# Optimization experiments

Measured on AMD Instinct MI355X. Metric: run time of the kernel, lower is better.

Reference implementation:

```python
import jax, jax.numpy as jnp
import numpy as np

N_NODES = 100000


def gcn_conv(x, src, dst, W, b, n_nodes):
    # PyG GCNConv: h = X W; out[i] = sum_j norm_ij * h[j] + b, with self-loops
    # and symmetric normalization norm_ij = deg(i)^-1/2 * deg(j)^-1/2.
    h = x @ W  # [N, out]
    deg = jax.ops.segment_sum(jnp.ones_like(dst, dtype=h.dtype), dst, num_segments=n_nodes)
    dinv = jnp.where(deg > 0, jax.lax.rsqrt(deg), 0.0)
    norm = dinv[src] * dinv[dst]  # [E]
    msg = h[src] * norm[:, None]  # [E, out] gather + scale
    out = jax.ops.segment_sum(msg, dst, num_segments=n_nodes)  # scatter-add
    return out + b


def setup_inputs() -> dict:
    key = jax.random.key(0)
    k_x, k_e, k_w1, k_w2 = jax.random.split(key, 4)
    in_c, hid, out_c = 128, 64, 32
    x = jax.random.normal(k_x, (N_NODES, in_c), dtype=jnp.float32)
    edge_index = jax.random.randint(k_e, (2, 1600000), 0, N_NODES, dtype=jnp.int32)
    W1 = jax.random.normal(k_w1, (in_c, hid), dtype=jnp.float32) / np.sqrt(in_c)
    b1 = jnp.zeros((hid,), dtype=jnp.float32)
    W2 = jax.random.normal(k_w2, (hid, out_c), dtype=jnp.float32) / np.sqrt(hid)
    b2 = jnp.zeros((out_c,), dtype=jnp.float32)
    return {"x": x, "edge_index": edge_index, "W1": W1, "b1": b1, "W2": W2, "b2": b2}


def reference(x, edge_index, W1, b1, W2, b2):
    n = x.shape[0]
    # add self-loops (GCNConv default)
    loops = jnp.arange(n, dtype=edge_index.dtype)
    src = jnp.concatenate([edge_index[0], loops])
    dst = jnp.concatenate([edge_index[1], loops])
    # faithful to original forward: x = (x*x)/x
    x = (x * x) / x
    h = jax.nn.relu(gcn_conv(x, src, dst, W1, b1, n))
    return gcn_conv(h, src, dst, W2, b2, n)
```

## Files before the change

### kernel.cpp

```cpp
#include <hip/hip_runtime.h>
#include <hip/hip_fp16.h>


#define IN_C 128
#define HID 64
#define OUTC 32
#define BSH 9
#define BSZ 512
#define NSLOT 256
#define EPB 8192

typedef _Float16 half8 __attribute__((ext_vector_type(8)));
typedef float f32x4 __attribute__((ext_vector_type(4)));

static __host__ __device__ __forceinline__ size_t szt(int a) { return (size_t)a; }

__global__ __launch_bounds__(256) void k_hist(const int* __restrict__ dst, int E,
                                              int* __restrict__ hist) {
  __shared__ int h[NSLOT];
  int tid = threadIdx.x;
  h[tid] = 0;
  __syncthreads();
  int e0 = blockIdx.x * EPB;
  int e1 = min(e0 + EPB, E);
  for (int i = e0 + tid; i < e1; i += 256) atomicAdd(&h[dst[i] >> BSH], 1);
  __syncthreads();
  hist[blockIdx.x * NSLOT + tid] = h[tid];
}

__global__ __launch_bounds__(256) void k_scan_col(int* __restrict__ hist, int B,
                                                  int* __restrict__ bucket_count) {
  __shared__ int sc[256];
  int k = blockIdx.x, t = threadIdx.x;
  int v = (t < B) ? hist[t * NSLOT + k] : 0;
  sc[t] = v;
  __syncthreads();
  for (int o = 1; o < 256; o <<= 1) {
    int w = (t >= o) ? sc[t - o] : 0;
    __syncthreads();
    sc[t] += w;
    __syncthreads();
  }
  if (t < B) hist[t * NSLOT + k] = sc[t] - v;
  if (t == 255) bucket_count[k] = sc[255];
}

__global__ __launch_bounds__(256) void k_scan_base(const int* __restrict__ bucket_count,
                                                   int* __restrict__ bucket_base) {
  __shared__ int sc[256];
  int t = threadIdx.x;
  int v = bucket_count[t];
  sc[t] = v;
  __syncthreads();
  for (int o = 1; o < 256; o <<= 1) {
    int w = (t >= o) ? sc[t - o] : 0;
    __syncthreads();
    sc[t] += w;
    __syncthreads();
  }
  bucket_base[t] = sc[t] - v;
}

__global__ __launch_bounds__(256) void k_scatter(const int* __restrict__ src,
                                                 const int* __restrict__ dst, int E,
                                                 const int* __restrict__ hist,
                                                 const int* __restrict__ bucket_base,
                                                 int* __restrict__ bedges) {
  __shared__ int off[NSLOT];
  int tid = threadIdx.x;
  off[tid] = hist[blockIdx.x * NSLOT + tid] + bucket_base[tid];
  __syncthreads();
  int e0 = blockIdx.x * EPB;
  int e1 = min(e0 + EPB, E);
  for (int i = e0 + tid; i < e1; i += 256) {
    int d = dst[i], s = src[i];
    int p = atomicAdd(&off[d >> BSH], 1);
    bedges[p] = (s << BSH) | (d & (BSZ - 1));
  }
}

__global__ __launch_bounds__(256) void k_bucket(const int* __restrict__ bedges,
                                                const int* __restrict__ bucket_base,
                                                const int* __restrict__ bucket_count,
                                                int2* __restrict__ rd,
                                                float* __restrict__ dinv,
                                                int* __restrict__ csr, int N) {
  __shared__ int h[BSZ];
  __shared__ int pfx[BSZ];
  __shared__ int cnt[BSZ];
  __shared__ int sc[256];
  int tid = threadIdx.x;
  int b = blockIdx.x;
  int base = bucket_base[b];
  int nE = bucket_count[b];
  h[tid] = 0; h[tid + 256] = 0;
  cnt[tid] = 0; cnt[tid + 256] = 0;
  __syncthreads();
  for (int i = tid; i < nE; i += 256) atomicAdd(&h[bedges[base + i] & (BSZ - 1)], 1);
  __syncthreads();
  int a0 = h[2 * tid], a1 = h[2 * tid + 1];
  int s = a0 + a1;
  sc[tid] = s;
  __syncthreads();
  for (int o = 1; o < 256; o <<= 1) {
    int v = (tid >= o) ? sc[tid - o] : 0;
    __syncthreads();
    sc[tid] += v;
    __syncthreads();
  }
  int ex = sc[tid] - s;
  pfx[2 * tid] = ex;
  pfx[2 * tid + 1] = ex + a0;
  __syncthreads();
  for (int i = tid; i < BSZ; i += 256) {
    int node = b * BSZ + i;
    if (node < N) {
      int dg = h[i];
      rd[node] = make_int2(base + pfx[i], dg);
      dinv[node] = rsqrtf((float)(dg + 1));
    }
  }
  for (int i = tid; i < nE; i += 256) {
    int e = bedges[base + i];
    int l = e & (BSZ - 1);
    int p = pfx[l] + atomicAdd(&cnt[l], 1);
    csr[base + p] = e >> BSH;
  }
}

__global__ __launch_bounds__(256) void k_gemm1(
    const float* __restrict__ x, const float* __restrict__ W1,
    const float* __restrict__ dinv, __half* __restrict__ h1s, int N) {
  __shared__ _Float16 bf[4 * 4 * 64 * 8];
  const int tid = threadIdx.x;
  for (int idx = tid; idx < 128 * 64; idx += 256) {
    int k = idx >> 6, c = idx & 63;
    int kc = k >> 5, kk = k & 31;
    int chunk = kk >> 3, j = kk & 7;
    int ct = c >> 4, cl = c & 15;
    bf[(((kc * 4 + ct) * 64) + chunk * 16 + cl) * 8 + j] = (_Float16)W1[idx];
  }
  __syncthreads();

  const int lane = tid & 63, wave = tid >> 6;
  const int row0 = blockIdx.x * 64 + wave * 16;
  const int r_a = lane & 15;
  const int chk = lane >> 4;
  const int arow = min(row0 + r_a, N - 1);
  const float* xp = x + szt(arow) * IN_C + chk * 8;

  f32x4 acc[4];
  #pragma unroll
  for (int ct = 0; ct < 4; ++ct) acc[ct] = (f32x4){0.f, 0.f, 0.f, 0.f};

  #pragma unroll
  for (int kc = 0; kc < 4; ++kc) {
    float4 a0 = *reinterpret_cast<const float4*>(xp + kc * 32);
    float4 a1v = *reinterpret_cast<const float4*>(xp + kc * 32 + 4);
    half8 af;
    af[0] = (_Float16)a0.x;  af[1] = (_Float16)a0.y;
    af[2] = (_Float16)a0.z;  af[3] = (_Float16)a0.w;
    af[4] = (_Float16)a1v.x; af[5] = (_Float16)a1v.y;
    af[6] = (_Float16)a1v.z; af[7] = (_Float16)a1v.w;
    #pragma unroll
    for (int ct = 0; ct < 4; ++ct) {
      half8 bfrag = *reinterpret_cast<const half8*>(&bf[(((kc * 4 + ct) * 64) + lane) * 8]);
      acc[ct] = __builtin_amdgcn_mfma_f32_16x16x32_f16(af, bfrag, acc[ct], 0, 0, 0);
    }
  }
  #pragma unroll
  for (int r = 0; r < 4; ++r) {
    int drow = row0 + chk * 4 + r;
    if (drow < N) {
      float di = dinv[drow];
      #pragma unroll
      for (int ct = 0; ct < 4; ++ct)
        h1s[szt(drow) * HID + ct * 16 + r_a] = (__half)(acc[ct][r] * di);
    }
  }
}

__global__ __launch_bounds__(256) void k_agg1(
    const __half* __restrict__ h1s, const int* __restrict__ csr,
    const int2* __restrict__ rd, const float* __restrict__ dinv,
    const float* __restrict__ b1, __half* __restrict__ a1, int N) {
  const int tid = threadIdx.x;
  int node = blockIdx.x * 32 + (tid >> 3);
  if (node >= N) return;
  const int l = tid & 7;
  const int g0 = (tid & 63) & ~7;
  const _Float16* hp = (const _Float16*)h1s;

  half8 selfv = *reinterpret_cast<const half8*>(hp + szt(node) * HID + l * 8);
  float acc[8];
  #pragma unroll
  for (int q = 0; q < 8; ++q) acc[q] = (float)selfv[q];

  int2 v = rd[node];
  int base = v.x, cnt = v.y;
  if (cnt > 0) {
    int last = base + cnt - 1;
    int myidx = csr[min(base + l, last)];
    for (int j = 0; j < cnt; j += 8) {
      int id[8];
      #pragma unroll
      for (int u = 0; u < 8; ++u) id[u] = __shfl(myidx, g0 + u);
      half8 gv[8];
      #pragma unroll
      for (int u = 0; u < 8; ++u)
        gv[u] = *reinterpret_cast<const half8*>(hp + szt(id[u]) * HID + l * 8);
      int jn = j + 8;
      if (jn < cnt) myidx = csr[min(base + jn + l, last)];
      #pragma unroll
      for (int u = 0; u < 8; ++u) {
        bool ok = (j + u) < cnt;
        #pragma unroll
        for (int q = 0; q < 8; ++q) acc[q] += ok ? (float)gv[u][q] : 0.0f;
      }
    }
  }
  float di = dinv[node];
  float4 bb0 = *reinterpret_cast<const float4*>(b1 + l * 8);
  float4 bb1 = *reinterpret_cast<const float4*>(b1 + l * 8 + 4);
  half8 o;
  o[0] = (_Float16)fmaxf(di * acc[0] + bb0.x, 0.f);
  o[1] = (_Float16)fmaxf(di * acc[1] + bb0.y, 0.f);
  o[2] = (_Float16)fmaxf(di * acc[2] + bb0.z, 0.f);
  o[3] = (_Float16)fmaxf(di * acc[3] + bb0.w, 0.f);
  o[4] = (_Float16)fmaxf(di * acc[4] + bb1.x, 0.f);
  o[5] = (_Float16)fmaxf(di * acc[5] + bb1.y, 0.f);
  o[6] = (_Float16)fmaxf(di * acc[6] + bb1.z, 0.f);
  o[7] = (_Float16)fmaxf(di * acc[7] + bb1.w, 0.f);
  *reinterpret_cast<half8*>((_Float16*)a1 + szt(node) * HID + l * 8) = o;
}

__global__ __launch_bounds__(256) void k_gemm2(
    const __half* __restrict__ a1, const float* __restrict__ W2,
    const float* __restrict__ dinv, __half* __restrict__ h2s, int N) {
  __shared__ _Float16 bf[2 * 2 * 64 * 8];
  const int tid = threadIdx.x;
  for (int idx = tid; idx < 64 * 32; idx += 256) {
    int k = idx >> 5, c = idx & 31;
    int kc = k >> 5, kk = k & 31;
    int chunk = kk >> 3, j = kk & 7;
    int ct = c >> 4, cl = c & 15;
    bf[(((kc * 2 + ct) * 64) + chunk * 16 + cl) * 8 + j] = (_Float16)W2[idx];
  }
  __syncthreads();

  const int lane = tid & 63, wave = tid >> 6;
  const int row0 = blockIdx.x * 64 + wave * 16;
  const int r_a = lane & 15;
  const int chk = lane >> 4;
  const int arow = min(row0 + r_a, N - 1);
  const _Float16* ap = (const _Float16*)a1 + szt(arow) * HID + chk * 8;

  f32x4 acc[2];
  acc[0] = (f32x4){0.f, 0.f, 0.f, 0.f};
  acc[1] = (f32x4){0.f, 0.f, 0.f, 0.f};
  #pragma unroll
  for (int kc = 0; kc < 2; ++kc) {
    half8 af = *reinterpret_cast<const half8*>(ap + kc * 32);
    #pragma unroll
    for (int ct = 0; ct < 2; ++ct) {
      half8 bfrag = *reinterpret_cast<const half8*>(&bf[(((kc * 2 + ct) * 64) + lane) * 8]);
      acc[ct] = __builtin_amdgcn_mfma_f32_16x16x32_f16(af, bfrag, acc[ct], 0, 0, 0);
    }
  }
  #pragma unroll
  for (int r = 0; r < 4; ++r) {
    int drow = row0 + chk * 4 + r;
    if (drow < N) {
      float di = dinv[drow];
      #pragma unroll
      for (int ct = 0; ct < 2; ++ct)
        h2s[szt(drow) * OUTC + ct * 16 + r_a] = (__half)(acc[ct][r] * di);
    }
  }
}

__global__ __launch_bounds__(256) void k_agg2(
    const __half* __restrict__ h2s, const int* __restrict__ csr,
    const int2* __restrict__ rd, const float* __restrict__ dinv,
    const float* __restrict__ b2, float* __restrict__ out, int N) {
  const int tid = threadIdx.x;
  int node = blockIdx.x * 64 + (tid >> 2);
  if (node >= N) return;
  const int l = tid & 3;
  const int g0 = (tid & 63) & ~3;
  const _Float16* hp = (const _Float16*)h2s;

  half8 selfv = *reinterpret_cast<const half8*>(hp + szt(node) * OUTC + l * 8);
  float acc[8];
  #pragma unroll
  for (int q = 0; q < 8; ++q) acc[q] = (float)selfv[q];

  int2 v = rd[node];
  int base = v.x, cnt = v.y;
  if (cnt > 0) {
    int last = base + cnt - 1;
    int myA = csr[min(base + 2 * l, last)];
    int myB = csr[min(base + 2 * l + 1, last)];
    for (int j = 0; j < cnt; j += 8) {
      int id[8];
      #pragma unroll
      for (int u = 0; u < 4; ++u) {
        id[2 * u]     = __shfl(myA, g0 + u);
        id[2 * u + 1] = __shfl(myB, g0 + u);
      }
      half8 gv[8];
      #pragma unroll
      for (int u = 0; u < 8; ++u)
        gv[u] = *reinterpret_cast<const half8*>(hp + szt(id[u]) * OUTC + l * 8);
      int jn = j + 8;
      if (jn < cnt) {
        myA = csr[min(base + jn + 2 * l, last)];
        myB = csr[min(base + jn + 2 * l + 1, last)];
      }
      #pragma unroll
      for (int u = 0; u < 8; ++u) {
        bool ok = (j + u) < cnt;
        #pragma unroll
        for (int q = 0; q < 8; ++q) acc[q] += ok ? (float)gv[u][q] : 0.0f;
      }
    }
  }
  float di = dinv[node];
  float4 bb0 = *reinterpret_cast<const float4*>(b2 + l * 8);
  float4 bb1 = *reinterpret_cast<const float4*>(b2 + l * 8 + 4);
  float4 o0, o1;
  o0.x = di * acc[0] + bb0.x; o0.y = di * acc[1] + bb0.y;
  o0.z = di * acc[2] + bb0.z; o0.w = di * acc[3] + bb0.w;
  o1.x = di * acc[4] + bb1.x; o1.y = di * acc[5] + bb1.y;
  o1.z = di * acc[6] + bb1.z; o1.w = di * acc[7] + bb1.w;
  float* op = out + szt(node) * OUTC + l * 8;
  *reinterpret_cast<float4*>(op) = o0;
  *reinterpret_cast<float4*>(op + 4) = o1;
}

extern "C" void kernel_launch(void* const* d_in, const int* in_sizes, int n_in,
                              void* d_out, int out_size, void* d_ws, size_t ws_size,
                              hipStream_t stream) {
  const float* x  = (const float*)d_in[0];
  const int*   ei = (const int*)d_in[1];
  const float* W1 = (const float*)d_in[2];
  const float* b1 = (const float*)d_in[3];
  const float* W2 = (const float*)d_in[4];
  const float* b2 = (const float*)d_in[5];
  float* out = (float*)d_out;

  const int N = in_sizes[0] / IN_C;
  const int E = in_sizes[1] / 2;
  const int* src = ei;
  const int* dst = ei + E;

  const int B  = (E + EPB - 1) / EPB;
  const int K1 = (N + BSZ - 1) / BSZ;

  char* ws = (char*)d_ws;
  size_t off = 0;
  auto alloc = [&](size_t bytes) {
    off = (off + 255) & ~(size_t)255;
    void* p = ws + off;
    off += bytes;
    return p;
  };
  int*    hist   = (int*)alloc(szt(B) * NSLOT * 4);
  int*    bbase  = (int*)alloc(NSLOT * 4);
  int*    bcount = (int*)alloc(NSLOT * 4);
  int2*   rd     = (int2*)alloc(szt(N) * 8);
  float*  dinv   = (float*)alloc(szt(N) * 4);
  int*    bedges = (int*)alloc(szt(E) * 4);
  int*    csr    = (int*)alloc(szt(E) * 4);
  __half* h1s    = (__half*)alloc(szt(N) * HID * 2);
  __half* a1     = (__half*)alloc(szt(N) * HID * 2);
  __half* h2s    = (__half*)alloc(szt(N) * OUTC * 2);
  (void)ws_size;

  k_hist<<<B, 256, 0, stream>>>(dst, E, hist);
  k_scan_col<<<NSLOT, 256, 0, stream>>>(hist, B, bcount);
  k_scan_base<<<1, 256, 0, stream>>>(bcount, bbase);
  k_scatter<<<B, 256, 0, stream>>>(src, dst, E, hist, bbase, bedges);
  k_bucket<<<K1, 256, 0, stream>>>(bedges, bbase, bcount, rd, dinv, csr, N);
  k_gemm1<<<(N + 63) / 64, 256, 0, stream>>>(x, W1, dinv, h1s, N);
  k_agg1<<<(N + 31) / 32, 256, 0, stream>>>(h1s, csr, rd, dinv, b1, a1, N);
  k_gemm2<<<(N + 63) / 64, 256, 0, stream>>>(a1, W2, dinv, h2s, N);
  k_agg2<<<(N + 63) / 64, 256, 0, stream>>>(h2s, csr, rd, dinv, b2, out, N);
}
```

Measured before the change: 127.4 us.

## Fold bucket-base scan into consumers, double EPB, widen aggregation gather to 16

Removes the single-block k_scan_base launch by having k_scatter and k_bucket each recompute the 256-entry exclusive scan of bucket counts in shared memory. Doubles edges per block in the histogram and scatter kernels, which halves the number of per-block histograms. Widens both aggregation loops to gather 16 neighbor rows per iteration for more memory-level parallelism, at the cost of more registers and more wasted lanes on low-degree nodes.

```diff
diff --git a/kernel.cpp b/kernel.cpp
--- a/kernel.cpp
+++ b/kernel.cpp
@@ -8,7 +8,7 @@
 #define BSH 9
 #define BSZ 512
 #define NSLOT 256
-#define EPB 8192
+#define EPB 16384
 
 typedef _Float16 half8 __attribute__((ext_vector_type(8)));
 typedef float f32x4 __attribute__((ext_vector_type(4)));
@@ -45,30 +45,24 @@
   if (t == 255) bucket_count[k] = sc[255];
 }
 
-__global__ __launch_bounds__(256) void k_scan_base(const int* __restrict__ bucket_count,
-                                                   int* __restrict__ bucket_base) {
-  __shared__ int sc[256];
-  int t = threadIdx.x;
-  int v = bucket_count[t];
-  sc[t] = v;
-  __syncthreads();
-  for (int o = 1; o < 256; o <<= 1) {
-    int w = (t >= o) ? sc[t - o] : 0;
-    __syncthreads();
-    sc[t] += w;
-    __syncthreads();
-  }
-  bucket_base[t] = sc[t] - v;
-}
-
 __global__ __launch_bounds__(256) void k_scatter(const int* __restrict__ src,
                                                  const int* __restrict__ dst, int E,
                                                  const int* __restrict__ hist,
-                                                 const int* __restrict__ bucket_base,
+                                                 const int* __restrict__ bucket_count,
                                                  int* __restrict__ bedges) {
   __shared__ int off[NSLOT];
+  __shared__ int sc[NSLOT];
   int tid = threadIdx.x;
-  off[tid] = hist[blockIdx.x * NSLOT + tid] + bucket_base[tid];
+  int v = bucket_count[tid];
+  sc[tid] = v;
+  __syncthreads();
+  for (int o = 1; o < 256; o <<= 1) {
+    int w = (tid >= o) ? sc[tid - o] : 0;
+    __syncthreads();
+    sc[tid] += w;
+    __syncthreads();
+  }
+  off[tid] = hist[blockIdx.x * NSLOT + tid] + (sc[tid] - v);
   __syncthreads();
   int e0 = blockIdx.x * EPB;
   int e1 = min(e0 + EPB, E);
@@ -80,7 +74,6 @@
 }
 
 __global__ __launch_bounds__(256) void k_bucket(const int* __restrict__ bedges,
-                                                const int* __restrict__ bucket_base,
                                                 const int* __restrict__ bucket_count,
                                                 int2* __restrict__ rd,
                                                 float* __restrict__ dinv,
@@ -89,9 +82,23 @@
   __shared__ int pfx[BSZ];
   __shared__ int cnt[BSZ];
   __shared__ int sc[256];
+  __shared__ int s_base;
   int tid = threadIdx.x;
   int b = blockIdx.x;
-  int base = bucket_base[b];
+  {
+    int v = bucket_count[tid];
+    sc[tid] = v;
+    __syncthreads();
+    for (int o = 1; o < 256; o <<= 1) {
+      int w = (tid >= o) ? sc[tid - o] : 0;
+      __syncthreads();
+      sc[tid] += w;
+      __syncthreads();
+    }
+    if (tid == b) s_base = sc[tid] - v;
+    __syncthreads();
+  }
+  int base = s_base;
   int nE = bucket_count[b];
   h[tid] = 0; h[tid + 256] = 0;
   cnt[tid] = 0; cnt[tid + 256] = 0;
@@ -200,19 +207,26 @@
   int base = v.x, cnt = v.y;
   if (cnt > 0) {
     int last = base + cnt - 1;
-    int myidx = csr[min(base + l, last)];
-    for (int j = 0; j < cnt; j += 8) {
-      int id[8];
-      #pragma unroll
-      for (int u = 0; u < 8; ++u) id[u] = __shfl(myidx, g0 + u);
-      half8 gv[8];
-      #pragma unroll
-      for (int u = 0; u < 8; ++u)
+    int myA = csr[min(base + l, last)];
+    int myB = csr[min(base + 8 + l, last)];
+    for (int j = 0; j < cnt; j += 16) {
+      int id[16];
+      #pragma unroll
+      for (int u = 0; u < 8; ++u) {
+        id[u] = __shfl(myA, g0 + u);
+        id[8 + u] = __shfl(myB, g0 + u);
+      }
+      half8 gv[16];
+      #pragma unroll
+      for (int u = 0; u < 16; ++u)
         gv[u] = *reinterpret_cast<const half8*>(hp + szt(id[u]) * HID + l * 8);
-      int jn = j + 8;
-      if (jn < cnt) myidx = csr[min(base + jn + l, last)];
-      #pragma unroll
-      for (int u = 0; u < 8; ++u) {
+      int jn = j + 16;
+      if (jn < cnt) {
+        myA = csr[min(base + jn + l, last)];
+        myB = csr[min(base + jn + 8 + l, last)];
+      }
+      #pragma unroll
+      for (int u = 0; u < 16; ++u) {
         bool ok = (j + u) < cnt;
         #pragma unroll
         for (int q = 0; q < 8; ++q) acc[q] += ok ? (float)gv[u][q] : 0.0f;
@@ -299,26 +313,32 @@
   int base = v.x, cnt = v.y;
   if (cnt > 0) {
     int last = base + cnt - 1;
-    int myA = csr[min(base + 2 * l, last)];
-    int myB = csr[min(base + 2 * l + 1, last)];
-    for (int j = 0; j < cnt; j += 8) {
-      int id[8];
+    int myA = csr[min(base + l, last)];
+    int myB = csr[min(base + 4 + l, last)];
+    int myC = csr[min(base + 8 + l, last)];
+    int myD = csr[min(base + 12 + l, last)];
+    for (int j = 0; j < cnt; j += 16) {
+      int id[16];
       #pragma unroll
       for (int u = 0; u < 4; ++u) {
-        id[2 * u]     = __shfl(myA, g0 + u);
-        id[2 * u + 1] = __shfl(myB, g0 + u);
-      }
-      half8 gv[8];
-      #pragma unroll
-      for (int u = 0; u < 8; ++u)
+        id[u]      = __shfl(myA, g0 + u);
+        id[4 + u]  = __shfl(myB, g0 + u);
+        id[8 + u]  = __shfl(myC, g0 + u);
+        id[12 + u] = __shfl(myD, g0 + u);
+      }
+      half8 gv[16];
+      #pragma unroll
+      for (int u = 0; u < 16; ++u)
         gv[u] = *reinterpret_cast<const half8*>(hp + szt(id[u]) * OUTC + l * 8);
-      int jn = j + 8;
+      int jn = j + 16;
       if (jn < cnt) {
-        myA = csr[min(base + jn + 2 * l, last)];
-        myB = csr[min(base + jn + 2 * l + 1, last)];
-      }
-      #pragma unroll
-      for (int u = 0; u < 8; ++u) {
+        myA = csr[min(base + jn + l, last)];
+        myB = csr[min(base + jn + 4 + l, last)];
+        myC = csr[min(base + jn + 8 + l, last)];
+        myD = csr[min(base + jn + 12 + l, last)];
+      }
+      #pragma unroll
+      for (int u = 0; u < 16; ++u) {
         bool ok = (j + u) < cnt;
         #pragma unroll
         for (int q = 0; q < 8; ++q) acc[q] += ok ? (float)gv[u][q] : 0.0f;
@@ -366,7 +386,6 @@
     return p;
   };
   int*    hist   = (int*)alloc(szt(B) * NSLOT * 4);
-  int*    bbase  = (int*)alloc(NSLOT * 4);
   int*    bcount = (int*)alloc(NSLOT * 4);
   int2*   rd     = (int2*)alloc(szt(N) * 8);
   float*  dinv   = (float*)alloc(szt(N) * 4);
@@ -379,9 +398,8 @@
 
   k_hist<<<B, 256, 0, stream>>>(dst, E, hist);
   k_scan_col<<<NSLOT, 256, 0, stream>>>(hist, B, bcount);
-  k_scan_base<<<1, 256, 0, stream>>>(bcount, bbase);
-  k_scatter<<<B, 256, 0, stream>>>(src, dst, E, hist, bbase, bedges);
-  k_bucket<<<K1, 256, 0, stream>>>(bedges, bbase, bcount, rd, dinv, csr, N);
+  k_scatter<<<B, 256, 0, stream>>>(src, dst, E, hist, bcount, bedges);
+  k_bucket<<<K1, 256, 0, stream>>>(bedges, bcount, rd, dinv, csr, N);
   k_gemm1<<<(N + 63) / 64, 256, 0, stream>>>(x, W1, dinv, h1s, N);
   k_agg1<<<(N + 31) / 32, 256, 0, stream>>>(h1s, csr, rd, dinv, b1, a1, N);
   k_gemm2<<<(N + 63) / 64, 256, 0, stream>>>(a1, W2, dinv, h2s, N);
```

New measurement: 144.8 us. +13.6%, slower.
